# Kernel optimization log

Measured on AMD Instinct MI355X. Metric: run time of the kernel, lower is better.

## Reference

```python
import jax, jax.numpy as jnp
import numpy as np

B, N, D, H, K, T = 32, 4096, 256, 4, 8, 3
D_H = D // H
SCALE = D_H ** -0.5
EPS = 1e-8
LN_EPS = 1e-5


def _ln(x, g, b):
    m = x.mean(-1, keepdims=True)
    v = ((x - m) ** 2).mean(-1, keepdims=True)
    return (x - m) / jnp.sqrt(v + LN_EPS) * g + b


def _split(t):  # [b, n, D] -> [b, H, n, d_h]
    b, n, _ = t.shape
    return t.reshape(b, n, H, D_H).transpose(0, 2, 1, 3)


def _merge(t):  # [b, H, n, d_h] -> [b, n, D]
    b, h, n, d = t.shape
    return t.transpose(0, 2, 1, 3).reshape(b, n, h * d)


def setup_inputs() -> dict:
    key = jax.random.key(0)
    ks = jax.random.split(key, 12)
    init = lambda k, shape: (jax.random.normal(k, shape, jnp.float32) * 0.02)
    mu = jnp.tile(jnp.linspace(-1.0, 1.0, K)[:, None], (1, D))[None]  # [1,K,D]
    return {
        'x': jax.random.normal(ks[0], (B, N, D), jnp.float32),
        'mu': mu,
        'w_q': init(ks[1], (D, D)),
        'w_k': init(ks[2], (D, D)),
        'w_v': init(ks[3], (D, D)),
        'w_comb': init(ks[4], (D, D)),
        'g_in': jnp.ones(D), 'b_in': jnp.zeros(D),
        'g_slot': jnp.ones(D), 'b_slot': jnp.zeros(D),
        'g_mlp': jnp.ones(D), 'b_mlp': jnp.zeros(D),
        'w_ih': init(ks[5], (3 * D, D)),
        'w_hh': init(ks[6], (3 * D, D)),
        'b_ih': jnp.zeros(3 * D),
        'b_hh': jnp.zeros(3 * D),
        'w1': init(ks[7], (D, D)), 'b1': jnp.zeros(D),
        'w2': init(ks[8], (D, D)), 'b2': jnp.zeros(D),
    }


def reference(x, mu, w_q, w_k, w_v, w_comb, g_in, b_in, g_slot, b_slot,
              g_mlp, b_mlp, w_ih, w_hh, b_ih, b_hh, w1, b1, w2, b2):
    b = x.shape[0]
    x_norm = _ln(x, g_in, b_in)
    k_feat = _split(x_norm @ w_k.T)  # [b,H,N,d_h]
    v_feat = _split(x_norm @ w_v.T)

    def gru(u, h):  # torch GRUCell semantics
        gi = u @ w_ih.T + b_ih
        gh = h @ w_hh.T + b_hh
        ir, iz, i_n = jnp.split(gi, 3, axis=-1)
        hr, hz, h_n = jnp.split(gh, 3, axis=-1)
        r = jax.nn.sigmoid(ir + hr)
        z = jax.nn.sigmoid(iz + hz)
        n = jnp.tanh(i_n + r * h_n)
        return (1.0 - z) * n + z * h

    def step(slots, _):
        q = _split(_ln(slots, g_slot, b_slot) @ w_q.T)  # [b,H,K,d_h]
        dots = jnp.einsum('bhkd,bhnd->bhkn', q, k_feat) * SCALE
        attn = jax.nn.softmax(dots, axis=-2)  # softmax over slots
        attn = attn / (attn.sum(axis=-1, keepdims=True) + EPS)  # renorm over inputs
        updates = _merge(jnp.einsum('bhkn,bhnd->bhkd', attn, v_feat)) @ w_comb.T
        new = gru(updates.reshape(-1, D), slots.reshape(-1, D)).reshape(slots.shape)
        hid = jnp.maximum(_ln(new, g_mlp, b_mlp) @ w1.T + b1, 0.0)
        new = new + (hid @ w2.T + b2)
        return new, None

    slots0 = jnp.broadcast_to(mu, (b, K, D))  # eval mode: slots = mu
    slots, _ = jax.lax.scan(step, slots0, None, length=T)
    return slots
```

## Files before the change

kernel.cpp:

```cpp
#include <hip/hip_runtime.h>

#define BB 32
#define NN 4096
#define DD 256
#define HH 4
#define KK 8
#define DH 64

typedef unsigned short u16;
typedef unsigned int u32;
typedef __attribute__((ext_vector_type(8))) short short8;
typedef __attribute__((ext_vector_type(4))) float f32x4;

__device__ __forceinline__ float b2f(u16 u){ return __uint_as_float(((u32)u)<<16); }
__device__ __forceinline__ u16 f2b(float f){
  u32 u = __float_as_uint(f);
  u32 r = (u + 0x7fffu + ((u>>16)&1u)) >> 16;
  return (u16)r;
}

__global__ __launch_bounds__(256) void prep_kernel(
    const float* __restrict__ mu, const float* __restrict__ w_q,
    const float* __restrict__ w_k, const float* __restrict__ w_v,
    const float* __restrict__ w_comb, const float* __restrict__ w_ih,
    const float* __restrict__ w_hh, const float* __restrict__ w1,
    const float* __restrict__ w2,
    u16* __restrict__ wkv, u16* __restrict__ wq_b, u16* __restrict__ wcomb_b,
    u16* __restrict__ wih_b, u16* __restrict__ whh_b, u16* __restrict__ w1_b,
    u16* __restrict__ w2_b, float* __restrict__ slots)
{
  int i = blockIdx.x*256 + threadIdx.x;
  if (i < 131072) {
    int c = i>>8, d = i&255;
    float v = (c<256) ? w_k[c*256+d] : w_v[(c-256)*256+d];
    int off = (c<<9) + ((2*d) ^ ((c&15)<<4));
    wkv[off>>1] = f2b(v);
    return;
  }
  i -= 131072;
  if (i < 65536){ wq_b[i] = f2b(w_q[i]); return; } i -= 65536;
  if (i < 65536){ wcomb_b[i] = f2b(w_comb[i]); return; } i -= 65536;
  if (i < 196608){ wih_b[i] = f2b(w_ih[i]); return; } i -= 196608;
  if (i < 196608){ whh_b[i] = f2b(w_hh[i]); return; } i -= 196608;
  if (i < 65536){ w1_b[i] = f2b(w1[i]); return; } i -= 65536;
  if (i < 65536){ w2_b[i] = f2b(w2[i]); return; } i -= 65536;
  if (i < 65536){ slots[i] = mu[i & 2047]; return; }
}

__global__ __launch_bounds__(512) void kv_proj_kernel(
    const float* __restrict__ x, const float* __restrict__ g_in,
    const float* __restrict__ b_in, const u16* __restrict__ wkv,
    u16* __restrict__ Kmat, u16* __restrict__ Vmat)
{
  __shared__ __align__(16) u16 Atile[64*256];
  __shared__ __align__(16) u16 Btile[64*256];
  __shared__ __align__(16) u16 Cbuf[64*64];
  const int tid = threadIdx.x;
  const int w = tid>>6, l = tid&63;
  const long row0 = (long)blockIdx.x * 64;

  short8 breg[4];
  #pragma unroll
  for (int i=0;i<4;++i)
    breg[i] = *(const short8*)((const char*)wkv + (i*512 + tid)*16);

  const f32x4 gv = *(const f32x4*)(g_in + l*4);
  const f32x4 bv = *(const f32x4*)(b_in + l*4);

  #pragma unroll
  for (int rr=0; rr<8; ++rr) {
    const int r = w*8 + rr;
    const f32x4 xv = *(const f32x4*)(x + (row0+r)*DD + l*4);
    float s = xv.x+xv.y+xv.z+xv.w;
    float s2 = xv.x*xv.x+xv.y*xv.y+xv.z*xv.z+xv.w*xv.w;
    #pragma unroll
    for (int m=1;m<64;m<<=1){ s += __shfl_xor(s,m); s2 += __shfl_xor(s2,m); }
    const float mean = s * (1.f/256.f);
    const float rstd = rsqrtf(s2*(1.f/256.f) - mean*mean + 1e-5f);
    const u32 p0 = (u32)f2b((xv.x-mean)*rstd*gv.x + bv.x) | ((u32)f2b((xv.y-mean)*rstd*gv.y + bv.y)<<16);
    const u32 p1 = (u32)f2b((xv.z-mean)*rstd*gv.z + bv.z) | ((u32)f2b((xv.w-mean)*rstd*gv.w + bv.w)<<16);
    const unsigned long long pp = (unsigned long long)p0 | ((unsigned long long)p1<<32);
    *(unsigned long long*)((char*)Atile + r*512 + ((l*8) ^ ((r&15)<<4))) = pp;
  }
  #pragma unroll
  for (int i=0;i<4;++i)
    *(short8*)((char*)Btile + (i*512+tid)*16) = breg[i];
  __syncthreads();

  const int wm = w>>2, wn = w&3;
  const int lr = l&15;
  const int lk = (l>>4)*8;

  for (int ct=0; ct<8; ++ct) {
    short8 nreg[4];
    if (ct < 7) {
      #pragma unroll
      for (int i=0;i<4;++i)
        nreg[i] = *(const short8*)((const char*)wkv + (ct+1)*32768 + (i*512 + tid)*16);
    }

    f32x4 acc0 = (f32x4)0.f, acc1 = (f32x4)0.f;
    #pragma unroll
    for (int ks=0; ks<8; ++ks) {
      const int k2 = (ks*32 + lk)*2;
      short8 af0, af1, bfv;
      { const int r = wm*32 + lr;       af0 = *(const short8*)((const char*)Atile + r*512 + (k2 ^ ((r&15)<<4))); }
      { const int r = wm*32 + 16 + lr;  af1 = *(const short8*)((const char*)Atile + r*512 + (k2 ^ ((r&15)<<4))); }
      { const int c = wn*16 + lr;       bfv = *(const short8*)((const char*)Btile + c*512 + (k2 ^ ((c&15)<<4))); }
      acc0 = __builtin_amdgcn_mfma_f32_16x16x32_bf16(af0, bfv, acc0, 0,0,0);
      acc1 = __builtin_amdgcn_mfma_f32_16x16x32_bf16(af1, bfv, acc1, 0,0,0);
    }

    {
      const int c = wn*16 + lr;
      #pragma unroll
      for (int reg=0; reg<4; ++reg) {
        const int r0r = wm*32 + (l>>4)*4 + reg;
        const int r1r = r0r + 16;
        *(u16*)((char*)Cbuf + r0r*128 + ((2*c) ^ ((r0r&7)<<4))) = f2b(acc0[reg]);
        *(u16*)((char*)Cbuf + r1r*128 + ((2*c) ^ ((r1r&7)<<4))) = f2b(acc1[reg]);
      }
    }
    __syncthreads();

    if (ct < 7) {
      #pragma unroll
      for (int i=0;i<4;++i)
        *(short8*)((char*)Btile + (i*512+tid)*16) = nreg[i];
    }
    {
      const int r = tid>>3, cg = tid&7;
      const short8 vv = *(const short8*)((char*)Cbuf + r*128 + ((cg*16) ^ ((r&7)<<4)));
      u16* dst = (ct<4) ? Kmat : Vmat;
      *(short8*)(dst + (row0+r)*DD + (ct&3)*64 + cg*8) = vv;
    }
    __syncthreads();
  }
}

__global__ __launch_bounds__(256) void slot_q_kernel(
    const float* __restrict__ slots, const float* __restrict__ g_slot,
    const float* __restrict__ b_slot, const u16* __restrict__ wq_b,
    float* __restrict__ qmat)
{
  __shared__ float xn[256];
  __shared__ float red[8];
  const int r = blockIdx.x, t = threadIdx.x;
  const int w = t>>6, l = t&63;
  const float xv = slots[r*256 + t];
  float s = xv, s2 = xv*xv;
  #pragma unroll
  for (int m=1;m<64;m<<=1){ s += __shfl_xor(s,m); s2 += __shfl_xor(s2,m); }
  if (l==0){ red[w*2]=s; red[w*2+1]=s2; }
  __syncthreads();
  s = red[0]+red[2]+red[4]+red[6];
  s2 = red[1]+red[3]+red[5]+red[7];
  const float mean = s*(1.f/256.f);
  const float rstd = rsqrtf(s2*(1.f/256.f)-mean*mean + 1e-5f);
  xn[t] = (xv-mean)*rstd*g_slot[t] + b_slot[t];
  __syncthreads();
  const u16* wr = wq_b + t*256;
  float a0=0,a1=0,a2=0,a3=0;
  for (int d=0; d<256; d+=8) {
    const short8 wv = *(const short8*)(wr + d);
    a0 = fmaf(b2f((u16)wv[0]), xn[d+0], a0);
    a1 = fmaf(b2f((u16)wv[1]), xn[d+1], a1);
    a2 = fmaf(b2f((u16)wv[2]), xn[d+2], a2);
    a3 = fmaf(b2f((u16)wv[3]), xn[d+3], a3);
    a0 = fmaf(b2f((u16)wv[4]), xn[d+4], a0);
    a1 = fmaf(b2f((u16)wv[5]), xn[d+5], a1);
    a2 = fmaf(b2f((u16)wv[6]), xn[d+6], a2);
    a3 = fmaf(b2f((u16)wv[7]), xn[d+7], a3);
  }
  qmat[r*256 + t] = ((a0+a1)+(a2+a3));
}

__global__ __launch_bounds__(256) void attn_kernel(
    const u16* __restrict__ Kmat, const u16* __restrict__ Vmat,
    const float* __restrict__ qmat, float* __restrict__ U_part,
    float* __restrict__ S_part)
{
  __shared__ float U_lds[4][8][64];
  __shared__ float S_lds[4][8];
  const int bid = blockIdx.x;
  const int part = bid & 3, h = (bid>>2)&3, b = bid>>4;
  const int t = threadIdx.x, w = t>>6, l = t&63;
  const int ds = l&7, ng = l>>3;

  float qreg[8][8];
  #pragma unroll
  for (int k=0;k<8;++k) {
    const f32x4 qa = *(const f32x4*)(qmat + (b*8+k)*256 + h*64 + ds*8);
    const f32x4 qb = *(const f32x4*)(qmat + (b*8+k)*256 + h*64 + ds*8 + 4);
    qreg[k][0]=qa.x; qreg[k][1]=qa.y; qreg[k][2]=qa.z; qreg[k][3]=qa.w;
    qreg[k][4]=qb.x; qreg[k][5]=qb.y; qreg[k][6]=qb.z; qreg[k][7]=qb.w;
  }

  float accU[8][8];
  float sacc[8];
  #pragma unroll
  for (int k=0;k<8;++k){ sacc[k]=0.f;
    #pragma unroll
    for (int j=0;j<8;++j) accU[k][j]=0.f; }

  const long base = ((long)b*NN)*DD + h*64;
  for (int pass=0; pass<32; ++pass) {
    const int n = part*1024 + pass*32 + w*8 + ng;
    const short8 kvv = *(const short8*)(Kmat + base + (long)n*DD + ds*8);
    float kd[8];
    #pragma unroll
    for (int j=0;j<8;++j) kd[j] = b2f((u16)kvv[j]);
    float dots[8];
    #pragma unroll
    for (int k=0;k<8;++k) {
      float d0 = qreg[k][0]*kd[0] + qreg[k][1]*kd[1] + qreg[k][2]*kd[2] + qreg[k][3]*kd[3]
               + qreg[k][4]*kd[4] + qreg[k][5]*kd[5] + qreg[k][6]*kd[6] + qreg[k][7]*kd[7];
      d0 += __shfl_xor(d0,1); d0 += __shfl_xor(d0,2); d0 += __shfl_xor(d0,4);
      dots[k] = d0 * 0.125f;
    }
    float mx = dots[0];
    #pragma unroll
    for (int k=1;k<8;++k) mx = fmaxf(mx, dots[k]);
    float e[8]; float se = 0.f;
    #pragma unroll
    for (int k=0;k<8;++k){ e[k] = __expf(dots[k]-mx); se += e[k]; }
    const float inv = 1.f/se;
    const short8 vvv = *(const short8*)(Vmat + base + (long)n*DD + ds*8);
    float vd[8];
    #pragma unroll
    for (int j=0;j<8;++j) vd[j] = b2f((u16)vvv[j]);
    #pragma unroll
    for (int k=0;k<8;++k) {
      const float p = e[k]*inv;
      sacc[k] += p;
      #pragma unroll
      for (int j=0;j<8;++j) accU[k][j] = fmaf(p, vd[j], accU[k][j]);
    }
  }
  #pragma unroll
  for (int k=0;k<8;++k){
    #pragma unroll
    for (int j=0;j<8;++j){
      float v = accU[k][j];
      v += __shfl_xor(v,8); v += __shfl_xor(v,16); v += __shfl_xor(v,32);
      accU[k][j]=v;
    }
    float sv = sacc[k];
    sv += __shfl_xor(sv,8); sv += __shfl_xor(sv,16); sv += __shfl_xor(sv,32);
    sacc[k]=sv;
  }
  if (l<8){
    #pragma unroll
    for (int k=0;k<8;++k)
      #pragma unroll
      for (int j=0;j<8;++j) U_lds[w][k][l*8+j] = accU[k][j];
  }
  if (l==0){
    #pragma unroll
    for (int k=0;k<8;++k) S_lds[w][k]=sacc[k];
  }
  __syncthreads();
  for (int i=t;i<512;i+=256){
    const int k=i>>6, d=i&63;
    U_part[(((long)part*32 + b)*4 + h)*512 + k*64 + d] =
      U_lds[0][k][d]+U_lds[1][k][d]+U_lds[2][k][d]+U_lds[3][k][d];
  }
  if (t<8){
    S_part[((part*32 + b)*4 + h)*8 + t] = S_lds[0][t]+S_lds[1][t]+S_lds[2][t]+S_lds[3][t];
  }
}

__global__ __launch_bounds__(256) void slot_update_kernel(
    const float* __restrict__ U_part, const float* __restrict__ S_part,
    float* __restrict__ slots,
    const u16* __restrict__ wcomb_b, const u16* __restrict__ wih_b,
    const u16* __restrict__ whh_b, const u16* __restrict__ w1_b,
    const u16* __restrict__ w2_b,
    const float* __restrict__ b_ih, const float* __restrict__ b_hh,
    const float* __restrict__ g_mlp, const float* __restrict__ b_mlp,
    const float* __restrict__ b1v, const float* __restrict__ b2v,
    float* __restrict__ out_final, const int write_out)
{
  __shared__ float uL[2][256];
  __shared__ float hL[2][256];
  __shared__ float cL[2][256];
  __shared__ float xL[2][256];
  __shared__ float red[16];
  const int blk = blockIdx.x, t = threadIdx.x;
  const int w = t>>6, l = t&63;
  const int r0 = blk*2;

  #pragma unroll
  for (int rr=0;rr<2;++rr) hL[rr][t] = slots[(r0+rr)*256 + t];

  #pragma unroll
  for (int rr=0;rr<2;++rr) {
    const int r = r0+rr, b = r>>3, k = r&7;
    const int h = t>>6, d = t&63;
    float ssum = 0.f, usum = 0.f;
    #pragma unroll
    for (int p=0;p<4;++p) {
      ssum += S_part[((p*32 + b)*4 + h)*8 + k];
      usum += U_part[(((long)p*32 + b)*4 + h)*512 + k*64 + d];
    }
    uL[rr][t] = usum / (ssum + 1e-8f);
  }
  __syncthreads();

  {
    float c00=0,c01=0,c10=0,c11=0;
    const u16* wr = wcomb_b + t*256;
    for (int d0=0; d0<256; d0+=8) {
      const short8 wv = *(const short8*)(wr + d0);
      float wf[8];
      #pragma unroll
      for (int j=0;j<8;++j) wf[j]=b2f((u16)wv[j]);
      #pragma unroll
      for (int j=0;j<8;j+=2) {
        c00 = fmaf(wf[j],   uL[0][d0+j],   c00);
        c01 = fmaf(wf[j+1], uL[0][d0+j+1], c01);
        c10 = fmaf(wf[j],   uL[1][d0+j],   c10);
        c11 = fmaf(wf[j+1], uL[1][d0+j+1], c11);
      }
    }
    cL[0][t]=c00+c01; cL[1][t]=c10+c11;
  }
  __syncthreads();

  float gi[3][2], gh[3][2];
  #pragma unroll
  for (int g=0; g<3; ++g){ gi[g][0]=0; gi[g][1]=0; gh[g][0]=0; gh[g][1]=0; }
  for (int d0=0; d0<256; d0+=8) {
    float u0[8],u1[8],h0[8],h1[8];
    #pragma unroll
    for (int j=0;j<8;j+=4) {
      *(f32x4*)&u0[j] = *(const f32x4*)&cL[0][d0+j];
      *(f32x4*)&u1[j] = *(const f32x4*)&cL[1][d0+j];
      *(f32x4*)&h0[j] = *(const f32x4*)&hL[0][d0+j];
      *(f32x4*)&h1[j] = *(const f32x4*)&hL[1][d0+j];
    }
    #pragma unroll
    for (int g=0; g<3; ++g) {
      const short8 wi = *(const short8*)(wih_b + (g*256+t)*256 + d0);
      const short8 wh = *(const short8*)(whh_b + (g*256+t)*256 + d0);
      #pragma unroll
      for (int j=0;j<8;++j) {
        const float a = b2f((u16)wi[j]);
        const float bw = b2f((u16)wh[j]);
        gi[g][0] = fmaf(a, u0[j], gi[g][0]);
        gi[g][1] = fmaf(a, u1[j], gi[g][1]);
        gh[g][0] = fmaf(bw, h0[j], gh[g][0]);
        gh[g][1] = fmaf(bw, h1[j], gh[g][1]);
      }
    }
  }
  float newv[2];
  #pragma unroll
  for (int rr=0;rr<2;++rr) {
    const float ir = gi[0][rr] + b_ih[t];
    const float iz = gi[1][rr] + b_ih[256+t];
    const float inn= gi[2][rr] + b_ih[512+t];
    const float hr = gh[0][rr] + b_hh[t];
    const float hz = gh[1][rr] + b_hh[256+t];
    const float hn = gh[2][rr] + b_hh[512+t];
    const float rg = 1.f/(1.f + __expf(-(ir+hr)));
    const float zg = 1.f/(1.f + __expf(-(iz+hz)));
    float targ = inn + rg*hn;
    targ = fminf(fmaxf(targ, -15.f), 15.f);
    const float ex = __expf(2.f*targ);
    const float ng = (ex-1.f)/(ex+1.f);
    newv[rr] = (1.f-zg)*ng + zg*hL[rr][t];
  }

  float s0=newv[0], q0=newv[0]*newv[0], s1=newv[1], q1=newv[1]*newv[1];
  #pragma unroll
  for (int m=1;m<64;m<<=1){
    s0+=__shfl_xor(s0,m); q0+=__shfl_xor(q0,m);
    s1+=__shfl_xor(s1,m); q1+=__shfl_xor(q1,m);
  }
  if (l==0){ red[w*4]=s0; red[w*4+1]=q0; red[w*4+2]=s1; red[w*4+3]=q1; }
  __syncthreads();
  s0 = red[0]+red[4]+red[8]+red[12];
  q0 = red[1]+red[5]+red[9]+red[13];
  s1 = red[2]+red[6]+red[10]+red[14];
  q1 = red[3]+red[7]+red[11]+red[15];
  {
    const float m0 = s0*(1.f/256.f), m1 = s1*(1.f/256.f);
    const float r0v = rsqrtf(q0*(1.f/256.f)-m0*m0 + 1e-5f);
    const float r1v = rsqrtf(q1*(1.f/256.f)-m1*m1 + 1e-5f);
    xL[0][t] = (newv[0]-m0)*r0v*g_mlp[t] + b_mlp[t];
    xL[1][t] = (newv[1]-m1)*r1v*g_mlp[t] + b_mlp[t];
  }
  __syncthreads();

  {
    float c00=0,c01=0,c10=0,c11=0;
    const u16* wr = w1_b + t*256;
    for (int d0=0; d0<256; d0+=8) {
      const short8 wv = *(const short8*)(wr + d0);
      float wf[8];
      #pragma unroll
      for (int j=0;j<8;++j) wf[j]=b2f((u16)wv[j]);
      #pragma unroll
      for (int j=0;j<8;j+=2) {
        c00 = fmaf(wf[j],   xL[0][d0+j],   c00);
        c01 = fmaf(wf[j+1], xL[0][d0+j+1], c01);
        c10 = fmaf(wf[j],   xL[1][d0+j],   c10);
        c11 = fmaf(wf[j+1], xL[1][d0+j+1], c11);
      }
    }
    uL[0][t] = fmaxf(c00+c01 + b1v[t], 0.f);
    uL[1][t] = fmaxf(c10+c11 + b1v[t], 0.f);
  }
  __syncthreads();

  {
    float c00=0,c01=0,c10=0,c11=0;
    const u16* wr = w2_b + t*256;
    for (int d0=0; d0<256; d0+=8) {
      const short8 wv = *(const short8*)(wr + d0);
      float wf[8];
      #pragma unroll
      for (int j=0;j<8;++j) wf[j]=b2f((u16)wv[j]);
      #pragma unroll
      for (int j=0;j<8;j+=2) {
        c00 = fmaf(wf[j],   uL[0][d0+j],   c00);
        c01 = fmaf(wf[j+1], uL[0][d0+j+1], c01);
        c10 = fmaf(wf[j],   uL[1][d0+j],   c10);
        c11 = fmaf(wf[j+1], uL[1][d0+j+1], c11);
      }
    }
    const float o0 = newv[0] + c00+c01 + b2v[t];
    const float o1 = newv[1] + c10+c11 + b2v[t];
    slots[(r0+0)*256 + t] = o0;
    slots[(r0+1)*256 + t] = o1;
    if (write_out){
      out_final[(r0+0)*256 + t] = o0;
      out_final[(r0+1)*256 + t] = o1;
    }
  }
}

extern "C" void kernel_launch(void* const* d_in, const int* in_sizes, int n_in,
                              void* d_out, int out_size, void* d_ws, size_t ws_size,
                              hipStream_t stream)
{
  (void)in_sizes; (void)n_in; (void)out_size; (void)ws_size;
  const float* x      = (const float*)d_in[0];
  const float* mu     = (const float*)d_in[1];
  const float* w_q    = (const float*)d_in[2];
  const float* w_k    = (const float*)d_in[3];
  const float* w_v    = (const float*)d_in[4];
  const float* w_comb = (const float*)d_in[5];
  const float* g_in   = (const float*)d_in[6];
  const float* b_in   = (const float*)d_in[7];
  const float* g_slot = (const float*)d_in[8];
  const float* b_slot = (const float*)d_in[9];
  const float* g_mlp  = (const float*)d_in[10];
  const float* b_mlp  = (const float*)d_in[11];
  const float* w_ih   = (const float*)d_in[12];
  const float* w_hh   = (const float*)d_in[13];
  const float* b_ih   = (const float*)d_in[14];
  const float* b_hh   = (const float*)d_in[15];
  const float* w1     = (const float*)d_in[16];
  const float* b1     = (const float*)d_in[17];
  const float* w2     = (const float*)d_in[18];
  const float* b2     = (const float*)d_in[19];

  char* ws = (char*)d_ws;
  u16* Kmat    = (u16*)(ws + 0);
  u16* Vmat    = (u16*)(ws + 67108864);
  u16* wkv     = (u16*)(ws + 134217728);
  u16* wq_b    = (u16*)(ws + 134479872);
  u16* wcomb_b = (u16*)(ws + 134610944);
  u16* wih_b   = (u16*)(ws + 134742016);
  u16* whh_b   = (u16*)(ws + 135135232);
  u16* w1_b    = (u16*)(ws + 135528448);
  u16* w2_b    = (u16*)(ws + 135659520);
  float* slots = (float*)(ws + 135790592);
  float* qmat  = (float*)(ws + 136052736);
  float* U_part= (float*)(ws + 136314880);
  float* S_part= (float*)(ws + 137363456);

  hipLaunchKernelGGL(prep_kernel, dim3(3328), dim3(256), 0, stream,
                     mu, w_q, w_k, w_v, w_comb, w_ih, w_hh, w1, w2,
                     wkv, wq_b, wcomb_b, wih_b, whh_b, w1_b, w2_b, slots);
  hipLaunchKernelGGL(kv_proj_kernel, dim3(2048), dim3(512), 0, stream,
                     x, g_in, b_in, wkv, Kmat, Vmat);
  float* outp = (float*)d_out;
  for (int it=0; it<3; ++it) {
    hipLaunchKernelGGL(slot_q_kernel, dim3(256), dim3(256), 0, stream,
                       slots, g_slot, b_slot, wq_b, qmat);
    hipLaunchKernelGGL(attn_kernel, dim3(512), dim3(256), 0, stream,
                       Kmat, Vmat, qmat, U_part, S_part);
    hipLaunchKernelGGL(slot_update_kernel, dim3(128), dim3(256), 0, stream,
                       U_part, S_part, slots, wcomb_b, wih_b, whh_b, w1_b, w2_b,
                       b_ih, b_hh, g_mlp, b_mlp, b1, b2, outp, (it==2)?1:0);
  }
}
```

Before: 368.1 us.

## Split attention over more blocks, prefetch K/V, fuse slot-q into update kernel

The attention kernel now splits each (batch, head) over 8 sequence parts instead of 4, giving 1024 blocks, and software-prefetches the next K/V rows one pass ahead. The slot update kernel handles one slot row per 512-thread block, with each dot product split across two half-threads. It also computes the next iteration's LayerNorm and query projection in place, which removes the per-iteration slot_q launch. The aims are more parallelism, hidden load latency and fewer launches, at the cost of more partial sums to reduce and more LDS use.

```diff
diff --git a/kernel.cpp b/kernel.cpp
--- a/kernel.cpp
+++ b/kernel.cpp
@@ -17,6 +17,23 @@
   u32 u = __float_as_uint(f);
   u32 r = (u + 0x7fffu + ((u>>16)&1u)) >> 16;
   return (u16)r;
+}
+
+__device__ __forceinline__ float dot128(const u16* __restrict__ wr, const float* __restrict__ v){
+  float a0=0,a1=0,a2=0,a3=0;
+  #pragma unroll
+  for (int d=0; d<128; d+=8){
+    const short8 wv = *(const short8*)(wr+d);
+    a0 = fmaf(b2f((u16)wv[0]), v[d+0], a0);
+    a1 = fmaf(b2f((u16)wv[1]), v[d+1], a1);
+    a2 = fmaf(b2f((u16)wv[2]), v[d+2], a2);
+    a3 = fmaf(b2f((u16)wv[3]), v[d+3], a3);
+    a0 = fmaf(b2f((u16)wv[4]), v[d+4], a0);
+    a1 = fmaf(b2f((u16)wv[5]), v[d+5], a1);
+    a2 = fmaf(b2f((u16)wv[6]), v[d+6], a2);
+    a3 = fmaf(b2f((u16)wv[7]), v[d+7], a3);
+  }
+  return (a0+a1)+(a2+a3);
 }
 
 __global__ __launch_bounds__(256) void prep_kernel(
@@ -183,7 +200,7 @@
   __shared__ float U_lds[4][8][64];
   __shared__ float S_lds[4][8];
   const int bid = blockIdx.x;
-  const int part = bid & 3, h = (bid>>2)&3, b = bid>>4;
+  const int part = bid & 7, h = (bid>>3)&3, b = bid>>5;
   const int t = threadIdx.x, w = t>>6, l = t&63;
   const int ds = l&7, ng = l>>3;
 
@@ -204,12 +221,20 @@
     for (int j=0;j<8;++j) accU[k][j]=0.f; }
 
   const long base = ((long)b*NN)*DD + h*64;
-  for (int pass=0; pass<32; ++pass) {
-    const int n = part*1024 + pass*32 + w*8 + ng;
-    const short8 kvv = *(const short8*)(Kmat + base + (long)n*DD + ds*8);
+  const u16* Kp = Kmat + base + (long)(part*512 + w*8 + ng)*DD + ds*8;
+  const u16* Vp = Vmat + base + (long)(part*512 + w*8 + ng)*DD + ds*8;
+
+  short8 kc = *(const short8*)Kp;
+  short8 vc = *(const short8*)Vp;
+  for (int pass=0; pass<16; ++pass) {
+    short8 kn, vn;
+    if (pass < 15) {
+      kn = *(const short8*)(Kp + (pass+1)*32*DD);
+      vn = *(const short8*)(Vp + (pass+1)*32*DD);
+    }
     float kd[8];
     #pragma unroll
-    for (int j=0;j<8;++j) kd[j] = b2f((u16)kvv[j]);
+    for (int j=0;j<8;++j) kd[j] = b2f((u16)kc[j]);
     float dots[8];
     #pragma unroll
     for (int k=0;k<8;++k) {
@@ -225,10 +250,9 @@
     #pragma unroll
     for (int k=0;k<8;++k){ e[k] = __expf(dots[k]-mx); se += e[k]; }
     const float inv = 1.f/se;
-    const short8 vvv = *(const short8*)(Vmat + base + (long)n*DD + ds*8);
     float vd[8];
     #pragma unroll
-    for (int j=0;j<8;++j) vd[j] = b2f((u16)vvv[j]);
+    for (int j=0;j<8;++j) vd[j] = b2f((u16)vc[j]);
     #pragma unroll
     for (int k=0;k<8;++k) {
       const float p = e[k]*inv;
@@ -236,6 +260,7 @@
       #pragma unroll
       for (int j=0;j<8;++j) accU[k][j] = fmaf(p, vd[j], accU[k][j]);
     }
+    kc = kn; vc = vn;
   }
   #pragma unroll
   for (int k=0;k<8;++k){
@@ -270,7 +295,7 @@
   }
 }
 
-__global__ __launch_bounds__(256) void slot_update_kernel(
+__global__ __launch_bounds__(512) void slot_update_kernel(
     const float* __restrict__ U_part, const float* __restrict__ S_part,
     float* __restrict__ slots,
     const u16* __restrict__ wcomb_b, const u16* __restrict__ wih_b,
@@ -279,165 +304,107 @@
     const float* __restrict__ b_ih, const float* __restrict__ b_hh,
     const float* __restrict__ g_mlp, const float* __restrict__ b_mlp,
     const float* __restrict__ b1v, const float* __restrict__ b2v,
-    float* __restrict__ out_final, const int write_out)
-{
-  __shared__ float uL[2][256];
-  __shared__ float hL[2][256];
-  __shared__ float cL[2][256];
-  __shared__ float xL[2][256];
-  __shared__ float red[16];
-  const int blk = blockIdx.x, t = threadIdx.x;
+    const u16* __restrict__ wq_b, const float* __restrict__ g_slot,
+    const float* __restrict__ b_slot, float* __restrict__ qmat,
+    float* __restrict__ out_final, const int write_out, const int compute_q)
+{
+  __shared__ float hvec[256], uvec[256], cvec[256], xvec[256], nvec[256];
+  __shared__ float part2[2][256];
+  __shared__ float part6[6][2][256];
+  __shared__ float red[8];
+  const int r = blockIdx.x, t = threadIdx.x;
+  const int col = t&255, kh = t>>8;
   const int w = t>>6, l = t&63;
-  const int r0 = blk*2;
-
-  #pragma unroll
-  for (int rr=0;rr<2;++rr) hL[rr][t] = slots[(r0+rr)*256 + t];
-
-  #pragma unroll
-  for (int rr=0;rr<2;++rr) {
-    const int r = r0+rr, b = r>>3, k = r&7;
-    const int h = t>>6, d = t&63;
-    float ssum = 0.f, usum = 0.f;
-    #pragma unroll
-    for (int p=0;p<4;++p) {
-      ssum += S_part[((p*32 + b)*4 + h)*8 + k];
-      usum += U_part[(((long)p*32 + b)*4 + h)*512 + k*64 + d];
-    }
-    uL[rr][t] = usum / (ssum + 1e-8f);
-  }
-  __syncthreads();
-
-  {
-    float c00=0,c01=0,c10=0,c11=0;
-    const u16* wr = wcomb_b + t*256;
-    for (int d0=0; d0<256; d0+=8) {
-      const short8 wv = *(const short8*)(wr + d0);
-      float wf[8];
-      #pragma unroll
-      for (int j=0;j<8;++j) wf[j]=b2f((u16)wv[j]);
-      #pragma unroll
-      for (int j=0;j<8;j+=2) {
-        c00 = fmaf(wf[j],   uL[0][d0+j],   c00);
-        c01 = fmaf(wf[j+1], uL[0][d0+j+1], c01);
-        c10 = fmaf(wf[j],   uL[1][d0+j],   c10);
-        c11 = fmaf(wf[j+1], uL[1][d0+j+1], c11);
-      }
-    }
-    cL[0][t]=c00+c01; cL[1][t]=c10+c11;
-  }
-  __syncthreads();
-
-  float gi[3][2], gh[3][2];
-  #pragma unroll
-  for (int g=0; g<3; ++g){ gi[g][0]=0; gi[g][1]=0; gh[g][0]=0; gh[g][1]=0; }
-  for (int d0=0; d0<256; d0+=8) {
-    float u0[8],u1[8],h0[8],h1[8];
-    #pragma unroll
-    for (int j=0;j<8;j+=4) {
-      *(f32x4*)&u0[j] = *(const f32x4*)&cL[0][d0+j];
-      *(f32x4*)&u1[j] = *(const f32x4*)&cL[1][d0+j];
-      *(f32x4*)&h0[j] = *(const f32x4*)&hL[0][d0+j];
-      *(f32x4*)&h1[j] = *(const f32x4*)&hL[1][d0+j];
-    }
-    #pragma unroll
-    for (int g=0; g<3; ++g) {
-      const short8 wi = *(const short8*)(wih_b + (g*256+t)*256 + d0);
-      const short8 wh = *(const short8*)(whh_b + (g*256+t)*256 + d0);
-      #pragma unroll
-      for (int j=0;j<8;++j) {
-        const float a = b2f((u16)wi[j]);
-        const float bw = b2f((u16)wh[j]);
-        gi[g][0] = fmaf(a, u0[j], gi[g][0]);
-        gi[g][1] = fmaf(a, u1[j], gi[g][1]);
-        gh[g][0] = fmaf(bw, h0[j], gh[g][0]);
-        gh[g][1] = fmaf(bw, h1[j], gh[g][1]);
-      }
-    }
-  }
-  float newv[2];
-  #pragma unroll
-  for (int rr=0;rr<2;++rr) {
-    const float ir = gi[0][rr] + b_ih[t];
-    const float iz = gi[1][rr] + b_ih[256+t];
-    const float inn= gi[2][rr] + b_ih[512+t];
-    const float hr = gh[0][rr] + b_hh[t];
-    const float hz = gh[1][rr] + b_hh[256+t];
-    const float hn = gh[2][rr] + b_hh[512+t];
+
+  if (t < 256) {
+    hvec[col] = slots[r*256 + col];
+    const int b = r>>3, k = r&7, h = col>>6, d = col&63;
+    float ssum=0.f, usum=0.f;
+    #pragma unroll
+    for (int p=0;p<8;++p){
+      ssum += S_part[((p*32+b)*4+h)*8 + k];
+      usum += U_part[(((long)p*32+b)*4+h)*512 + k*64 + d];
+    }
+    uvec[col] = usum/(ssum + 1e-8f);
+  }
+  __syncthreads();
+
+  part2[kh][col] = dot128(wcomb_b + col*256 + kh*128, &uvec[kh*128]);
+  __syncthreads();
+  if (t<256) cvec[col] = part2[0][col] + part2[1][col];
+  __syncthreads();
+
+  part6[0][kh][col] = dot128(wih_b + (0*256+col)*256 + kh*128, &cvec[kh*128]);
+  part6[1][kh][col] = dot128(wih_b + (1*256+col)*256 + kh*128, &cvec[kh*128]);
+  part6[2][kh][col] = dot128(wih_b + (2*256+col)*256 + kh*128, &cvec[kh*128]);
+  part6[3][kh][col] = dot128(whh_b + (0*256+col)*256 + kh*128, &hvec[kh*128]);
+  part6[4][kh][col] = dot128(whh_b + (1*256+col)*256 + kh*128, &hvec[kh*128]);
+  part6[5][kh][col] = dot128(whh_b + (2*256+col)*256 + kh*128, &hvec[kh*128]);
+  __syncthreads();
+
+  float newv = 0.f;
+  if (t<256){
+    const float ir = part6[0][0][col]+part6[0][1][col] + b_ih[col];
+    const float iz = part6[1][0][col]+part6[1][1][col] + b_ih[256+col];
+    const float inn= part6[2][0][col]+part6[2][1][col] + b_ih[512+col];
+    const float hr = part6[3][0][col]+part6[3][1][col] + b_hh[col];
+    const float hz = part6[4][0][col]+part6[4][1][col] + b_hh[256+col];
+    const float hn = part6[5][0][col]+part6[5][1][col] + b_hh[512+col];
     const float rg = 1.f/(1.f + __expf(-(ir+hr)));
     const float zg = 1.f/(1.f + __expf(-(iz+hz)));
     float targ = inn + rg*hn;
     targ = fminf(fmaxf(targ, -15.f), 15.f);
     const float ex = __expf(2.f*targ);
     const float ng = (ex-1.f)/(ex+1.f);
-    newv[rr] = (1.f-zg)*ng + zg*hL[rr][t];
-  }
-
-  float s0=newv[0], q0=newv[0]*newv[0], s1=newv[1], q1=newv[1]*newv[1];
-  #pragma unroll
-  for (int m=1;m<64;m<<=1){
-    s0+=__shfl_xor(s0,m); q0+=__shfl_xor(q0,m);
-    s1+=__shfl_xor(s1,m); q1+=__shfl_xor(q1,m);
-  }
-  if (l==0){ red[w*4]=s0; red[w*4+1]=q0; red[w*4+2]=s1; red[w*4+3]=q1; }
-  __syncthreads();
-  s0 = red[0]+red[4]+red[8]+red[12];
-  q0 = red[1]+red[5]+red[9]+red[13];
-  s1 = red[2]+red[6]+red[10]+red[14];
-  q1 = red[3]+red[7]+red[11]+red[15];
-  {
-    const float m0 = s0*(1.f/256.f), m1 = s1*(1.f/256.f);
-    const float r0v = rsqrtf(q0*(1.f/256.f)-m0*m0 + 1e-5f);
-    const float r1v = rsqrtf(q1*(1.f/256.f)-m1*m1 + 1e-5f);
-    xL[0][t] = (newv[0]-m0)*r0v*g_mlp[t] + b_mlp[t];
-    xL[1][t] = (newv[1]-m1)*r1v*g_mlp[t] + b_mlp[t];
-  }
-  __syncthreads();
-
-  {
-    float c00=0,c01=0,c10=0,c11=0;
-    const u16* wr = w1_b + t*256;
-    for (int d0=0; d0<256; d0+=8) {
-      const short8 wv = *(const short8*)(wr + d0);
-      float wf[8];
-      #pragma unroll
-      for (int j=0;j<8;++j) wf[j]=b2f((u16)wv[j]);
-      #pragma unroll
-      for (int j=0;j<8;j+=2) {
-        c00 = fmaf(wf[j],   xL[0][d0+j],   c00);
-        c01 = fmaf(wf[j+1], xL[0][d0+j+1], c01);
-        c10 = fmaf(wf[j],   xL[1][d0+j],   c10);
-        c11 = fmaf(wf[j+1], xL[1][d0+j+1], c11);
-      }
-    }
-    uL[0][t] = fmaxf(c00+c01 + b1v[t], 0.f);
-    uL[1][t] = fmaxf(c10+c11 + b1v[t], 0.f);
-  }
-  __syncthreads();
-
-  {
-    float c00=0,c01=0,c10=0,c11=0;
-    const u16* wr = w2_b + t*256;
-    for (int d0=0; d0<256; d0+=8) {
-      const short8 wv = *(const short8*)(wr + d0);
-      float wf[8];
-      #pragma unroll
-      for (int j=0;j<8;++j) wf[j]=b2f((u16)wv[j]);
-      #pragma unroll
-      for (int j=0;j<8;j+=2) {
-        c00 = fmaf(wf[j],   uL[0][d0+j],   c00);
-        c01 = fmaf(wf[j+1], uL[0][d0+j+1], c01);
-        c10 = fmaf(wf[j],   uL[1][d0+j],   c10);
-        c11 = fmaf(wf[j+1], uL[1][d0+j+1], c11);
-      }
-    }
-    const float o0 = newv[0] + c00+c01 + b2v[t];
-    const float o1 = newv[1] + c10+c11 + b2v[t];
-    slots[(r0+0)*256 + t] = o0;
-    slots[(r0+1)*256 + t] = o1;
-    if (write_out){
-      out_final[(r0+0)*256 + t] = o0;
-      out_final[(r0+1)*256 + t] = o1;
-    }
+    newv = (1.f-zg)*ng + zg*hvec[col];
+    nvec[col] = newv;
+    float s = newv, s2 = newv*newv;
+    #pragma unroll
+    for (int m=1;m<64;m<<=1){ s += __shfl_xor(s,m); s2 += __shfl_xor(s2,m); }
+    if (l==0){ red[w*2]=s; red[w*2+1]=s2; }
+  }
+  __syncthreads();
+  if (t<256){
+    const float s  = red[0]+red[2]+red[4]+red[6];
+    const float s2 = red[1]+red[3]+red[5]+red[7];
+    const float mean = s*(1.f/256.f);
+    const float rstd = rsqrtf(s2*(1.f/256.f)-mean*mean + 1e-5f);
+    xvec[col] = (newv-mean)*rstd*g_mlp[col] + b_mlp[col];
+  }
+  __syncthreads();
+
+  part2[kh][col] = dot128(w1_b + col*256 + kh*128, &xvec[kh*128]);
+  __syncthreads();
+  if (t<256) cvec[col] = fmaxf(part2[0][col]+part2[1][col] + b1v[col], 0.f);
+  __syncthreads();
+
+  part2[kh][col] = dot128(w2_b + col*256 + kh*128, &cvec[kh*128]);
+  __syncthreads();
+  float o = 0.f;
+  if (t<256){
+    o = nvec[col] + part2[0][col]+part2[1][col] + b2v[col];
+    slots[r*256 + col] = o;
+    if (write_out) out_final[r*256 + col] = o;
+    if (compute_q){
+      float s = o, s2 = o*o;
+      #pragma unroll
+      for (int m=1;m<64;m<<=1){ s += __shfl_xor(s,m); s2 += __shfl_xor(s2,m); }
+      if (l==0){ red[w*2]=s; red[w*2+1]=s2; }
+    }
+  }
+  if (compute_q){
+    __syncthreads();
+    if (t<256){
+      const float s  = red[0]+red[2]+red[4]+red[6];
+      const float s2 = red[1]+red[3]+red[5]+red[7];
+      const float mean = s*(1.f/256.f);
+      const float rstd = rsqrtf(s2*(1.f/256.f)-mean*mean + 1e-5f);
+      xvec[col] = (o-mean)*rstd*g_slot[col] + b_slot[col];
+    }
+    __syncthreads();
+    part2[kh][col] = dot128(wq_b + col*256 + kh*128, &xvec[kh*128]);
+    __syncthreads();
+    if (t<256) qmat[r*256 + col] = part2[0][col] + part2[1][col];
   }
 }
 
@@ -480,21 +447,23 @@
   float* slots = (float*)(ws + 135790592);
   float* qmat  = (float*)(ws + 136052736);
   float* U_part= (float*)(ws + 136314880);
-  float* S_part= (float*)(ws + 137363456);
+  float* S_part= (float*)(ws + 138412032);
 
   hipLaunchKernelGGL(prep_kernel, dim3(3328), dim3(256), 0, stream,
                      mu, w_q, w_k, w_v, w_comb, w_ih, w_hh, w1, w2,
                      wkv, wq_b, wcomb_b, wih_b, whh_b, w1_b, w2_b, slots);
   hipLaunchKernelGGL(kv_proj_kernel, dim3(2048), dim3(512), 0, stream,
                      x, g_in, b_in, wkv, Kmat, Vmat);
+  hipLaunchKernelGGL(slot_q_kernel, dim3(256), dim3(256), 0, stream,
+                     slots, g_slot, b_slot, wq_b, qmat);
   float* outp = (float*)d_out;
   for (int it=0; it<3; ++it) {
-    hipLaunchKernelGGL(slot_q_kernel, dim3(256), dim3(256), 0, stream,
-                       slots, g_slot, b_slot, wq_b, qmat);
-    hipLaunchKernelGGL(attn_kernel, dim3(512), dim3(256), 0, stream,
+    hipLaunchKernelGGL(attn_kernel, dim3(1024), dim3(256), 0, stream,
                        Kmat, Vmat, qmat, U_part, S_part);
-    hipLaunchKernelGGL(slot_update_kernel, dim3(128), dim3(256), 0, stream,
+    hipLaunchKernelGGL(slot_update_kernel, dim3(256), dim3(512), 0, stream,
                        U_part, S_part, slots, wcomb_b, wih_b, whh_b, w1_b, w2_b,
-                       b_ih, b_hh, g_mlp, b_mlp, b1, b2, outp, (it==2)?1:0);
-  }
-}
+                       b_ih, b_hh, g_mlp, b_mlp, b1, b2,
+                       wq_b, g_slot, b_slot, qmat,
+                       outp, (it==2)?1:0, (it<2)?1:0);
+  }
+}
```

Measured after the change: 408.0 us. 1.11x slower.
